# Kernel optimization log

Measured on AMD Instinct MI355X. Metric: run time of the kernel, lower is better.

## Reference

```python
import jax, jax.numpy as jnp
import numpy as np

H = 31  # hidden_size == input_size


def setup_inputs() -> dict:
    key = jax.random.key(0)
    ks = jax.random.split(key, 7)
    B, T = 2048, 512
    s = 1.0 / np.sqrt(H)
    return {
        "x": jax.random.normal(ks[0], (B, T, H), dtype=jnp.float32),
        "W_ih": jax.random.uniform(ks[1], (3 * H, H), minval=-s, maxval=s, dtype=jnp.float32),
        "W_hh": jax.random.uniform(ks[2], (3 * H, H), minval=-s, maxval=s, dtype=jnp.float32),
        "b_ih": jax.random.uniform(ks[3], (3 * H,), minval=-s, maxval=s, dtype=jnp.float32),
        "b_hh": jax.random.uniform(ks[4], (3 * H,), minval=-s, maxval=s, dtype=jnp.float32),
        "W_fc": jax.random.uniform(ks[5], (2, H), minval=-s, maxval=s, dtype=jnp.float32),
        "b_fc": jax.random.uniform(ks[6], (2,), minval=-s, maxval=s, dtype=jnp.float32),
    }


def _gru_seq(x, W_ih, W_hh, b_ih, b_hh):
    # x: [B, T, I]. Precompute input-side gates for all timesteps (one big GEMM).
    B = x.shape[0]
    xg = jnp.einsum("bti,gi->btg", x, W_ih) + b_ih          # [B, T, 3H]
    xg = jnp.swapaxes(xg, 0, 1)                              # [T, B, 3H]

    def step(h, xg_t):
        gh = h @ W_hh.T + b_hh                               # [B, 3H]
        ir, iz, inn = jnp.split(xg_t, 3, axis=-1)
        hr, hz, hn = jnp.split(gh, 3, axis=-1)
        r = jax.nn.sigmoid(ir + hr)
        z = jax.nn.sigmoid(iz + hz)
        n = jnp.tanh(inn + r * hn)
        h_new = (1.0 - z) * n + z * h
        return h_new, h_new

    h0 = jnp.zeros((B, H), dtype=x.dtype)
    _, out = jax.lax.scan(step, h0, xg)                      # out: [T, B, H]
    return jnp.swapaxes(out, 0, 1)                           # [B, T, H]


def reference(x, W_ih, W_hh, b_ih, b_hh, W_fc, b_fc):
    out = _gru_seq(x, W_ih, W_hh, b_ih, b_hh)                # [B, T, H]
    return out @ W_fc.T + b_fc                               # [B, T, 2]
```

## Files before the change

### kernel.cpp

```cpp
#include <hip/hip_runtime.h>


constexpr int BB = 2048, TT = 512, HH = 31;
constexpr float LOG2E = 1.4426950408889634f;

typedef _Float16 hf8 __attribute__((ext_vector_type(8)));
typedef float f32x4 __attribute__((ext_vector_type(4)));

__device__ __forceinline__ float fast_exp2(float v) {
#if __has_builtin(__builtin_amdgcn_exp2f)
    return __builtin_amdgcn_exp2f(v);
#else
    return exp2f(v);
#endif
}
__device__ __forceinline__ float fast_rcp(float v) {
#if __has_builtin(__builtin_amdgcn_rcpf)
    return __builtin_amdgcn_rcpf(v);
#else
    return __fdividef(1.f, v);
#endif
}
__device__ __forceinline__ unsigned pk2(float a, float b) {
    return __builtin_bit_cast(unsigned, __builtin_amdgcn_cvt_pkrtz(a, b));
}

struct F8 { float v0, v1, v2, v3, v4, v5, v6, v7; };
__device__ __forceinline__ void ldx(F8* d, const float* p) {
    __builtin_memcpy(d, p, 32);
}

__global__ __launch_bounds__(64, 1) void gru_one_kernel(
    const float* __restrict__ x, const float* __restrict__ W_ih,
    const float* __restrict__ W_hh, const float* __restrict__ b_ih,
    const float* __restrict__ b_hh, const float* __restrict__ W_fc,
    const float* __restrict__ b_fc, float* __restrict__ out)
{
    const int lane  = threadIdx.x & 63;
    const int col   = lane & 15;
    const int grp   = lane >> 4;
    const int batch = blockIdx.x * 16 + col;

    hf8 Ah[6], Ax[6];
    {
        const int gp = col >> 2, jj = col & 3;
#pragma unroll
        for (int c = 0; c < 6; ++c) {
            const int q = 4 * c + jj, s = q / 3, m = q - 3 * s, u = 8 * gp + s;
#pragma unroll
            for (int e = 0; e < 8; ++e) {
                const int kh = 8 * grp + e;
                const int kx = kh - (grp == 3 ? 1 : 0);
                float vh = 0.f, vx = 0.f;
                if (u == 31) {
                    if (q == 22 && kh < HH) vh = W_fc[kh];
                    if (q == 23 && kh < HH) vh = W_fc[HH + kh];
                } else {
                    const float sc = (m == 2) ? 2.f * LOG2E : LOG2E;
                    const int row = 31 * m + u;
                    if (kh < HH) vh = sc * W_hh[row * HH + kh];
                    if (!(grp == 2 && e == 7)) vx = sc * W_ih[row * HH + kx];
                }
                Ah[c][e] = (_Float16)vh;
                Ax[c][e] = (_Float16)vx;
            }
        }
    }

    f32x4 Ch[6], Cx[6];
#pragma unroll
    for (int c = 0; c < 6; ++c)
#pragma unroll
        for (int j = 0; j < 4; ++j) {
            const int q = 4 * c + j, s = q / 3, m = q - 3 * s, u = 8 * grp + s;
            float vh = 0.f, vx = 0.f;
            if (u == 31) {
                if (q == 22) vh = b_fc[0];
                if (q == 23) vh = b_fc[1];
            } else {
                const float sc = (m == 2) ? 2.f * LOG2E : LOG2E;
                vh = sc * b_hh[31 * m + u];
                vx = sc * b_ih[31 * m + u];
            }
            Ch[c][j] = vh;
            Cx[c][j] = vx;
        }

    const float* xb  = x + (size_t)batch * TT * HH + (8 * grp - (grp == 3 ? 1 : 0));
    float*      outp = out + (size_t)batch * TT * 2;

    float h0 = 0.f, h1 = 0.f, h2 = 0.f, h3 = 0.f,
          h4 = 0.f, h5 = 0.f, h6 = 0.f, h7 = 0.f;
    int4 bhi = make_int4(0, 0, 0, 0);

    F8 xA, xB;
    ldx(&xA, xb);
    ldx(&xB, xb + HH);

#define GATE(ca,ja, cb,jb, cc,jc, H) { \
        const float pr  = Dh[ca][ja] + Dx[ca][ja]; \
        const float pz  = Dh[cb][jb] + Dx[cb][jb]; \
        const float pnh = Dh[cc][jc]; \
        const float xn  = Dx[cc][jc]; \
        const float r   = fast_rcp(1.f + fast_exp2(-pr)); \
        const float z   = fast_rcp(1.f + fast_exp2(-pz)); \
        const float en  = fast_exp2(-fmaf(r, pnh, xn)); \
        const float nn  = fmaf(2.f, fast_rcp(1.f + en), -1.f); \
        H = nn + z * (H - nn); \
    }

#define STEP_BODY(T, XS) { \
        const int4 bxi = make_int4(pk2(XS.v0, XS.v1), pk2(XS.v2, XS.v3), \
                                   pk2(XS.v4, XS.v5), pk2(XS.v6, XS.v7)); \
        const hf8 Bx = __builtin_bit_cast(hf8, bxi); \
        const hf8 Bh = __builtin_bit_cast(hf8, bhi); \
        f32x4 Dh[6], Dx[6]; \
        Dx[0] = __builtin_amdgcn_mfma_f32_16x16x32_f16(Ax[0], Bx, Cx[0], 0, 0, 0); \
        Dx[1] = __builtin_amdgcn_mfma_f32_16x16x32_f16(Ax[1], Bx, Cx[1], 0, 0, 0); \
        Dx[2] = __builtin_amdgcn_mfma_f32_16x16x32_f16(Ax[2], Bx, Cx[2], 0, 0, 0); \
        Dx[3] = __builtin_amdgcn_mfma_f32_16x16x32_f16(Ax[3], Bx, Cx[3], 0, 0, 0); \
        Dx[4] = __builtin_amdgcn_mfma_f32_16x16x32_f16(Ax[4], Bx, Cx[4], 0, 0, 0); \
        Dx[5] = __builtin_amdgcn_mfma_f32_16x16x32_f16(Ax[5], Bx, Cx[5], 0, 0, 0); \
        Dh[0] = __builtin_amdgcn_mfma_f32_16x16x32_f16(Ah[0], Bh, Ch[0], 0, 0, 0); \
        Dh[1] = __builtin_amdgcn_mfma_f32_16x16x32_f16(Ah[1], Bh, Ch[1], 0, 0, 0); \
        Dh[2] = __builtin_amdgcn_mfma_f32_16x16x32_f16(Ah[2], Bh, Ch[2], 0, 0, 0); \
        Dh[3] = __builtin_amdgcn_mfma_f32_16x16x32_f16(Ah[3], Bh, Ch[3], 0, 0, 0); \
        Dh[4] = __builtin_amdgcn_mfma_f32_16x16x32_f16(Ah[4], Bh, Ch[4], 0, 0, 0); \
        Dh[5] = __builtin_amdgcn_mfma_f32_16x16x32_f16(Ah[5], Bh, Ch[5], 0, 0, 0); \
        if (grp == 3 && (T) > 0) \
            *(float2*)(outp + (size_t)((T) - 1) * 2) = make_float2(Dh[5][2], Dh[5][3]); \
        GATE(0,0, 0,1, 0,2, h0)  GATE(0,3, 1,0, 1,1, h1) \
        GATE(1,2, 1,3, 2,0, h2)  GATE(2,1, 2,2, 2,3, h3) \
        GATE(3,0, 3,1, 3,2, h4)  GATE(3,3, 4,0, 4,1, h5) \
        GATE(4,2, 4,3, 5,0, h6)  GATE(5,1, 5,2, 5,3, h7) \
        if (grp == 3) h7 = 0.f;                       \
        bhi = make_int4(pk2(h0, h1), pk2(h2, h3), pk2(h4, h5), pk2(h6, h7)); \
    }

    for (int t = 0; t < TT; t += 2) {
        {
            const F8 xs = xA;
            if (t + 2 < TT) ldx(&xA, xb + (size_t)(t + 2) * HH);
            STEP_BODY(t, xs)
        }
        {
            const F8 xs = xB;
            if (t + 3 < TT) ldx(&xB, xb + (size_t)(t + 3) * HH);
            STEP_BODY(t + 1, xs)
        }
    }

    {
        const hf8 Bh = __builtin_bit_cast(hf8, bhi);
        const f32x4 D5 = __builtin_amdgcn_mfma_f32_16x16x32_f16(Ah[5], Bh, Ch[5], 0, 0, 0);
        if (grp == 3)
            *(float2*)(outp + (size_t)(TT - 1) * 2) = make_float2(D5[2], D5[3]);
    }
#undef STEP_BODY
#undef GATE
}

extern "C" void kernel_launch(void* const* d_in, const int* in_sizes, int n_in,
                              void* d_out, int out_size, void* d_ws, size_t ws_size,
                              hipStream_t stream) {
    const float* x    = (const float*)d_in[0];
    const float* W_ih = (const float*)d_in[1];
    const float* W_hh = (const float*)d_in[2];
    const float* b_ih = (const float*)d_in[3];
    const float* b_hh = (const float*)d_in[4];
    const float* W_fc = (const float*)d_in[5];
    const float* b_fc = (const float*)d_in[6];
    float* out = (float*)d_out;

    gru_one_kernel<<<BB / 16, 64, 0, stream>>>(x, W_ih, W_hh, b_ih, b_hh,
                                               W_fc, b_fc, out);
}
```

Baseline: 325.2 us.

## Chain x-side MFMA into h-side accumulator and share reciprocal for r,z gates

Reorders the gate rows so r, z and n each occupy whole MFMA tiles. For r and z, the x-projection result feeds the h-projection MFMA as its accumulator, so the h-side sum needs no separate add and the two biases are folded together. The r and z sigmoids share one reciprocal of the product of their denominators. The FC output is moved into the padded row-31 slots, which now go through the chained accumulator, and the final step issues two MFMAs instead of one. Chaining MFMAs puts the x-side MFMA latency on the dependent path, and the shared reciprocal may lose some accuracy.

```diff
diff --git a/kernel.cpp b/kernel.cpp
--- a/kernel.cpp
+++ b/kernel.cpp
@@ -46,20 +46,23 @@
         const int gp = col >> 2, jj = col & 3;
 #pragma unroll
         for (int c = 0; c < 6; ++c) {
-            const int q = 4 * c + jj, s = q / 3, m = q - 3 * s, u = 8 * gp + s;
+            const int base = (c >> 1);
+            const int u    = 8 * gp + 4 * (c & 1) + jj;
+            const bool fc0 = (base == 0 && u == 31);
+            const bool fc1 = (base == 1 && u == 31);
+            const bool pad = (base == 2 && u == 31);
+            const float sc = (base == 2) ? 2.f * LOG2E : LOG2E;
+            const int wrow = 31 * base + u;
 #pragma unroll
             for (int e = 0; e < 8; ++e) {
                 const int kh = 8 * grp + e;
                 const int kx = kh - (grp == 3 ? 1 : 0);
                 float vh = 0.f, vx = 0.f;
-                if (u == 31) {
-                    if (q == 22 && kh < HH) vh = W_fc[kh];
-                    if (q == 23 && kh < HH) vh = W_fc[HH + kh];
-                } else {
-                    const float sc = (m == 2) ? 2.f * LOG2E : LOG2E;
-                    const int row = 31 * m + u;
-                    if (kh < HH) vh = sc * W_hh[row * HH + kh];
-                    if (!(grp == 2 && e == 7)) vx = sc * W_ih[row * HH + kx];
+                if (fc0)      { if (kh < HH) vh = W_fc[kh]; }
+                else if (fc1) { if (kh < HH) vh = W_fc[HH + kh]; }
+                else if (!pad) {
+                    if (kh < HH) vh = sc * W_hh[wrow * HH + kh];
+                    if (!(grp == 2 && e == 7)) vx = sc * W_ih[wrow * HH + kx];
                 }
                 Ah[c][e] = (_Float16)vh;
                 Ax[c][e] = (_Float16)vx;
@@ -67,74 +70,80 @@
         }
     }
 
-    f32x4 Ch[6], Cx[6];
+    f32x4 Cx[6], Chn[2];
 #pragma unroll
     for (int c = 0; c < 6; ++c)
 #pragma unroll
         for (int j = 0; j < 4; ++j) {
-            const int q = 4 * c + j, s = q / 3, m = q - 3 * s, u = 8 * grp + s;
-            float vh = 0.f, vx = 0.f;
+            const int base = (c >> 1);
+            const int u    = 8 * grp + 4 * (c & 1) + j;
+            float vx = 0.f;
             if (u == 31) {
-                if (q == 22) vh = b_fc[0];
-                if (q == 23) vh = b_fc[1];
+                if (base == 0) vx = b_fc[0];
+                else if (base == 1) vx = b_fc[1];
+            } else if (base < 2) {
+                vx = LOG2E * (b_ih[31 * base + u] + b_hh[31 * base + u]);
             } else {
-                const float sc = (m == 2) ? 2.f * LOG2E : LOG2E;
-                vh = sc * b_hh[31 * m + u];
-                vx = sc * b_ih[31 * m + u];
+                vx = 2.f * LOG2E * b_ih[62 + u];
             }
-            Ch[c][j] = vh;
             Cx[c][j] = vx;
+            if (base == 2) Chn[c - 4][j] = (u == 31) ? 0.f : 2.f * LOG2E * b_hh[62 + u];
         }
 
     const float* xb  = x + (size_t)batch * TT * HH + (8 * grp - (grp == 3 ? 1 : 0));
     float*      outp = out + (size_t)batch * TT * 2;
 
-    float h0 = 0.f, h1 = 0.f, h2 = 0.f, h3 = 0.f,
-          h4 = 0.f, h5 = 0.f, h6 = 0.f, h7 = 0.f;
+    float hreg[8];
+#pragma unroll
+    for (int s = 0; s < 8; ++s) hreg[s] = 0.f;
     int4 bhi = make_int4(0, 0, 0, 0);
 
     F8 xA, xB;
     ldx(&xA, xb);
     ldx(&xB, xb + HH);
 
-#define GATE(ca,ja, cb,jb, cc,jc, H) { \
-        const float pr  = Dh[ca][ja] + Dx[ca][ja]; \
-        const float pz  = Dh[cb][jb] + Dx[cb][jb]; \
-        const float pnh = Dh[cc][jc]; \
-        const float xn  = Dx[cc][jc]; \
-        const float r   = fast_rcp(1.f + fast_exp2(-pr)); \
-        const float z   = fast_rcp(1.f + fast_exp2(-pz)); \
-        const float en  = fast_exp2(-fmaf(r, pnh, xn)); \
-        const float nn  = fmaf(2.f, fast_rcp(1.f + en), -1.f); \
-        H = nn + z * (H - nn); \
-    }
-
 #define STEP_BODY(T, XS) { \
         const int4 bxi = make_int4(pk2(XS.v0, XS.v1), pk2(XS.v2, XS.v3), \
                                    pk2(XS.v4, XS.v5), pk2(XS.v6, XS.v7)); \
         const hf8 Bx = __builtin_bit_cast(hf8, bxi); \
         const hf8 Bh = __builtin_bit_cast(hf8, bhi); \
-        f32x4 Dh[6], Dx[6]; \
+        f32x4 Dx[6], Dh[6]; \
         Dx[0] = __builtin_amdgcn_mfma_f32_16x16x32_f16(Ax[0], Bx, Cx[0], 0, 0, 0); \
         Dx[1] = __builtin_amdgcn_mfma_f32_16x16x32_f16(Ax[1], Bx, Cx[1], 0, 0, 0); \
         Dx[2] = __builtin_amdgcn_mfma_f32_16x16x32_f16(Ax[2], Bx, Cx[2], 0, 0, 0); \
         Dx[3] = __builtin_amdgcn_mfma_f32_16x16x32_f16(Ax[3], Bx, Cx[3], 0, 0, 0); \
         Dx[4] = __builtin_amdgcn_mfma_f32_16x16x32_f16(Ax[4], Bx, Cx[4], 0, 0, 0); \
         Dx[5] = __builtin_amdgcn_mfma_f32_16x16x32_f16(Ax[5], Bx, Cx[5], 0, 0, 0); \
-        Dh[0] = __builtin_amdgcn_mfma_f32_16x16x32_f16(Ah[0], Bh, Ch[0], 0, 0, 0); \
-        Dh[1] = __builtin_amdgcn_mfma_f32_16x16x32_f16(Ah[1], Bh, Ch[1], 0, 0, 0); \
-        Dh[2] = __builtin_amdgcn_mfma_f32_16x16x32_f16(Ah[2], Bh, Ch[2], 0, 0, 0); \
-        Dh[3] = __builtin_amdgcn_mfma_f32_16x16x32_f16(Ah[3], Bh, Ch[3], 0, 0, 0); \
-        Dh[4] = __builtin_amdgcn_mfma_f32_16x16x32_f16(Ah[4], Bh, Ch[4], 0, 0, 0); \
-        Dh[5] = __builtin_amdgcn_mfma_f32_16x16x32_f16(Ah[5], Bh, Ch[5], 0, 0, 0); \
+        Dh[0] = __builtin_amdgcn_mfma_f32_16x16x32_f16(Ah[0], Bh, Dx[0], 0, 0, 0); \
+        Dh[1] = __builtin_amdgcn_mfma_f32_16x16x32_f16(Ah[1], Bh, Dx[1], 0, 0, 0); \
+        Dh[2] = __builtin_amdgcn_mfma_f32_16x16x32_f16(Ah[2], Bh, Dx[2], 0, 0, 0); \
+        Dh[3] = __builtin_amdgcn_mfma_f32_16x16x32_f16(Ah[3], Bh, Dx[3], 0, 0, 0); \
+        Dh[4] = __builtin_amdgcn_mfma_f32_16x16x32_f16(Ah[4], Bh, Chn[0], 0, 0, 0); \
+        Dh[5] = __builtin_amdgcn_mfma_f32_16x16x32_f16(Ah[5], Bh, Chn[1], 0, 0, 0); \
         if (grp == 3 && (T) > 0) \
-            *(float2*)(outp + (size_t)((T) - 1) * 2) = make_float2(Dh[5][2], Dh[5][3]); \
-        GATE(0,0, 0,1, 0,2, h0)  GATE(0,3, 1,0, 1,1, h1) \
-        GATE(1,2, 1,3, 2,0, h2)  GATE(2,1, 2,2, 2,3, h3) \
-        GATE(3,0, 3,1, 3,2, h4)  GATE(3,3, 4,0, 4,1, h5) \
-        GATE(4,2, 4,3, 5,0, h6)  GATE(5,1, 5,2, 5,3, h7) \
-        if (grp == 3) h7 = 0.f;                       \
-        bhi = make_int4(pk2(h0, h1), pk2(h2, h3), pk2(h4, h5), pk2(h6, h7)); \
+            *(float2*)(outp + (size_t)((T) - 1) * 2) = make_float2(Dh[1][3], Dh[3][3]); \
+        float er[8], ez[8], aa[8], bb[8], RR[8], rr[8], zz[8], en[8], nv[8]; \
+        _Pragma("unroll") \
+        for (int s = 0; s < 8; ++s) { \
+            er[s] = fast_exp2(-Dh[s >> 2][s & 3]); \
+            ez[s] = fast_exp2(-Dh[2 + (s >> 2)][s & 3]); \
+        } \
+        _Pragma("unroll") \
+        for (int s = 0; s < 8; ++s) { aa[s] = 1.f + er[s]; bb[s] = 1.f + ez[s]; } \
+        _Pragma("unroll") \
+        for (int s = 0; s < 8; ++s) RR[s] = fast_rcp(aa[s] * bb[s]); \
+        _Pragma("unroll") \
+        for (int s = 0; s < 8; ++s) { rr[s] = bb[s] * RR[s]; zz[s] = aa[s] * RR[s]; } \
+        _Pragma("unroll") \
+        for (int s = 0; s < 8; ++s) \
+            en[s] = fast_exp2(-fmaf(rr[s], Dh[4 + (s >> 2)][s & 3], Dx[4 + (s >> 2)][s & 3])); \
+        _Pragma("unroll") \
+        for (int s = 0; s < 8; ++s) nv[s] = fmaf(2.f, fast_rcp(1.f + en[s]), -1.f); \
+        _Pragma("unroll") \
+        for (int s = 0; s < 8; ++s) hreg[s] = fmaf(zz[s], hreg[s] - nv[s], nv[s]); \
+        if (grp == 3) hreg[7] = 0.f;                  \
+        bhi = make_int4(pk2(hreg[0], hreg[1]), pk2(hreg[2], hreg[3]), \
+                        pk2(hreg[4], hreg[5]), pk2(hreg[6], hreg[7])); \
     }
 
     for (int t = 0; t < TT; t += 2) {
@@ -152,12 +161,12 @@
 
     {
         const hf8 Bh = __builtin_bit_cast(hf8, bhi);
-        const f32x4 D5 = __builtin_amdgcn_mfma_f32_16x16x32_f16(Ah[5], Bh, Ch[5], 0, 0, 0);
+        const f32x4 D1 = __builtin_amdgcn_mfma_f32_16x16x32_f16(Ah[1], Bh, Cx[1], 0, 0, 0);
+        const f32x4 D3 = __builtin_amdgcn_mfma_f32_16x16x32_f16(Ah[3], Bh, Cx[3], 0, 0, 0);
         if (grp == 3)
-            *(float2*)(outp + (size_t)(TT - 1) * 2) = make_float2(D5[2], D5[3]);
+            *(float2*)(outp + (size_t)(TT - 1) * 2) = make_float2(D1[3], D3[3]);
     }
 #undef STEP_BODY
-#undef GATE
 }
 
 extern "C" void kernel_launch(void* const* d_in, const int* in_sizes, int n_in,
```

After: 296.8 us. 1.1x faster.
